# Kernel tuning notes

Measured on AMD Instinct MI355X. Metric: run time of the kernel, lower is better.

Reference implementation:

```python
import jax, jax.numpy as jnp
import numpy as np

N_HEAD = 16


def setup_inputs() -> dict:
    key = jax.random.key(0)
    k1, k2, k3 = jax.random.split(key, 3)
    B, S, D = 4, 2048, 1024
    scale = 1.0 / np.sqrt(D)
    return {
        "inp": jax.random.normal(k1, (B, S, D), dtype=jnp.float32),
        "w_attn": jax.random.normal(k2, (D, 3 * D), dtype=jnp.float32) * scale,
        "b_attn": jnp.zeros((3 * D,), dtype=jnp.float32),
        "w_proj": jax.random.normal(k3, (D, D), dtype=jnp.float32) * scale,
        "b_proj": jnp.zeros((D,), dtype=jnp.float32),
    }


def reference(inp, w_attn, b_attn, w_proj, b_proj):
    B, S, D = inp.shape
    H = N_HEAD
    hd = D // H
    qkv = inp @ w_attn + b_attn                      # [B,S,3D]
    q, k, v = jnp.split(qkv, 3, axis=-1)
    q = q.reshape(B, S, H, hd)
    k = k.reshape(B, S, H, hd)
    v = v.reshape(B, S, H, hd)
    # scores [B,H,S,S], scaled by 1/sqrt(head_dim)
    scores = jnp.einsum("bqhd,bkhd->bhqk", q, k) / jnp.sqrt(jnp.asarray(hd, dtype=inp.dtype))
    # causal mask: position q attends to k <= q
    causal = jnp.tril(jnp.ones((S, S), dtype=bool))
    scores = jnp.where(causal[None, None], scores, jnp.asarray(-jnp.inf, dtype=scores.dtype))
    probs = jax.nn.softmax(scores, axis=-1)          # dropout omitted (eval mode)
    ctx = jnp.einsum("bhqk,bkhd->bqhd", probs, v).reshape(B, S, D)
    return ctx @ w_proj + b_proj
```

## Files before the change

### kernel.cpp

```cpp
#include <hip/hip_runtime.h>


#define DEV __device__ __forceinline__

typedef unsigned short u16;
typedef unsigned u32x4 __attribute__((ext_vector_type(4)));
typedef u16   u16x8 __attribute__((ext_vector_type(8)));
typedef u16   u16x4 __attribute__((ext_vector_type(4)));
typedef float f32x4v __attribute__((ext_vector_type(4)));
typedef __bf16 bf16x8 __attribute__((ext_vector_type(8)));

#define BB 4
#define SS 2048
#define DD 1024
#define HH 16
#define HD 64
#define MM (BB*SS)
#define N3D (3*DD)
#define C8  0.18033688011112042f

DEV u16 f2bf(float f) { return __builtin_bit_cast(u16, (__bf16)f); }
DEV float bf2f(u16 h) { return __builtin_bit_cast(float, (unsigned)h << 16); }

DEV f32x4v mfma16(u16x8 a, u16x8 b, f32x4v c) {
  return __builtin_amdgcn_mfma_f32_16x16x32_bf16(
      __builtin_bit_cast(bf16x8, a), __builtin_bit_cast(bf16x8, b), c, 0, 0, 0);
}

DEV void async16(const void* g, void* l) {
  __builtin_amdgcn_global_load_lds(
      (const __attribute__((address_space(1))) void*)g,
      (__attribute__((address_space(3))) void*)l, 16, 0, 0);
}

__global__ __launch_bounds__(256) void prep_kernel(
    const float* __restrict__ inp, const float* __restrict__ w_attn,
    const float* __restrict__ w_proj, u16* __restrict__ Abf,
    u16* __restrict__ WAt, u16* __restrict__ WPt) {
  const int bid = blockIdx.x;
  const int tid = threadIdx.x;
  if (bid < 4096) {
    __shared__ float t[32][33];
    const float* W; u16* Wt; int N, K, n0, k0;
    if (bid < 3072) { W = w_attn; Wt = WAt; N = N3D; K = DD;
                      n0 = (bid % 96) * 32; k0 = (bid / 96) * 32; }
    else            { W = w_proj; Wt = WPt; N = DD;  K = DD;
                      int tb = bid - 3072; n0 = (tb % 32) * 32; k0 = (tb / 32) * 32; }
    int tx = tid & 31, ty = tid >> 5;
    for (int i = ty; i < 32; i += 8)
      t[i][tx] = W[(long long)(k0 + i) * N + n0 + tx];
    __syncthreads();
    for (int i = ty; i < 32; i += 8)
      Wt[(long long)(n0 + i) * K + k0 + tx] = f2bf(t[tx][i]);
  } else {
    const long long n = (long long)MM * DD;
    long long i = (long long)(bid - 4096) * 256 + tid;
    for (long long j = i * 4; j < n; j += 2048LL * 256 * 4) {
      f32x4v v = *(const f32x4v*)(inp + j);
      u16x4 o;
      o.x = f2bf(v.x); o.y = f2bf(v.y); o.z = f2bf(v.z); o.w = f2bf(v.w);
      *(u16x4*)(Abf + j) = o;
    }
  }
}

__global__ __launch_bounds__(256) void gemm_kernel(
    const u16* __restrict__ A, const u16* __restrict__ Bt,
    const float* __restrict__ bias, void* __restrict__ Cout,
    u16* __restrict__ Vt, int Ndim, int Kdim, int mode) {
  __shared__ __align__(16) char smem[65536];

  const int tid = threadIdx.x;
  const int lane = tid & 63, wid = tid >> 6;
  const int l15 = lane & 15, lg = lane >> 4;

  const int nwg = (int)(gridDim.x * gridDim.y);
  const int orig = (int)(blockIdx.y * gridDim.x + blockIdx.x);
  const int wg = (orig & 7) * (nwg >> 3) + (orig >> 3);
  const int bx = wg % (int)gridDim.x, by = wg / (int)gridDim.x;
  const int rb = by * 128, cb = bx * 128;
  const int wr = (wid >> 1) * 64, wc = (wid & 1) * 64;

  f32x4v acc[4][4] = {};

  const int rlo = tid >> 3;
  const int cbS = (tid & 7) * 16;
  const int swS = cbS ^ ((rlo & 7) << 4);
  const int sd  = rlo * 128 + cbS;

  const int xr  = (l15 & 7) << 4;
  const int vaA = l15 * 128 + ((lg * 16) ^ xr);
  const int gvA0 = wr * 128 + vaA, gvA1 = gvA0 ^ 64;
  const int gvB0 = wc * 128 + vaA, gvB1 = gvB0 ^ 64;

  const char* pa[4];
  const char* pb[4];
#pragma unroll
  for (int i = 0; i < 4; ++i) {
    pa[i] = (const char*)A  + (long long)(rb + i * 32 + rlo) * (Kdim * 2) + swS;
    pb[i] = (const char*)Bt + (long long)(cb + i * 32 + rlo) * (Kdim * 2) + swS;
  }

  auto stage = [&](int dofs, int kb) {
#pragma unroll
    for (int i = 0; i < 4; ++i) {
      async16(pa[i] + kb, smem + dofs + i * 4096 + sd);
      async16(pb[i] + kb, smem + 32768 + dofs + i * 4096 + sd);
    }
  };

  auto compute = [&](int aofs, int bofs) {
    u16x8 a0[4], b0[4], a1[4], b1[4];
#pragma unroll
    for (int mi = 0; mi < 4; ++mi) {
      a0[mi] = *(const u16x8*)(smem + aofs + mi * 2048 + gvA0);
      a1[mi] = *(const u16x8*)(smem + aofs + mi * 2048 + gvA1);
    }
#pragma unroll
    for (int ni = 0; ni < 4; ++ni) {
      b0[ni] = *(const u16x8*)(smem + bofs + ni * 2048 + gvB0);
      b1[ni] = *(const u16x8*)(smem + bofs + ni * 2048 + gvB1);
    }
#pragma unroll
    for (int mi = 0; mi < 4; ++mi)
#pragma unroll
      for (int ni = 0; ni < 4; ++ni) {
        acc[mi][ni] = mfma16(a0[mi], b0[ni], acc[mi][ni]);
        acc[mi][ni] = mfma16(a1[mi], b1[ni], acc[mi][ni]);
      }
  };

  const int nK = Kdim >> 6;
  stage(0, 0);
  __syncthreads();
  for (int kt = 0; kt < nK; kt += 2) {
    stage(16384, 128);
    compute(0, 32768);
    __syncthreads();
    if (kt + 2 < nK) stage(0, 256);
    compute(16384, 49152);
    __syncthreads();
#pragma unroll
    for (int i = 0; i < 4; ++i) { pa[i] += 256; pb[i] += 256; }
  }

#pragma unroll
  for (int mi = 0; mi < 4; ++mi)
#pragma unroll
    for (int ni = 0; ni < 4; ++ni) {
      int col = cb + wc + ni * 16 + l15;
      float bv = bias[col];
      if (mode == 1 && col >= 2 * DD) {
        int h = (col >> 6) & 15, d = col & 63;
#pragma unroll
        for (int r = 0; r < 4; ++r) {
          int row = rb + wr + mi * 16 + lg * 4 + r;
          int b = row >> 11, s = row & 2047;
          Vt[(((long long)(b * HH + h) * HD + d) << 11) + s] = f2bf(acc[mi][ni][r] + bv);
        }
      } else {
#pragma unroll
        for (int r = 0; r < 4; ++r) {
          int row = rb + wr + mi * 16 + lg * 4 + r;
          float v = acc[mi][ni][r] + bv;
          if (mode) ((u16*)Cout)[(long long)row * Ndim + col] = f2bf(v);
          else      ((float*)Cout)[(long long)row * Ndim + col] = v;
        }
      }
    }
}

__global__ __launch_bounds__(512, 4) void attn_kernel(
    const u16* __restrict__ qkv, const u16* __restrict__ Vt,
    u16* __restrict__ ctx) {
  __shared__ __align__(16) char smem[32768];

  const int tid = threadIdx.x, lane = tid & 63, wid = tid >> 6;
  const int l15 = lane & 15, lg = lane >> 4;

  const int orig = (int)blockIdx.x;
  const int wgid = (orig & 7) * 64 + (orig >> 3);
  const int pair = wgid & 7;
  const int bh = wgid >> 3;
  const int b = bh >> 4, h = bh & 15;

  const u16* Qcol = qkv + (long long)b * SS * N3D + h * HD;
  const u16* Kcol = qkv + (long long)b * SS * N3D + DD + h * HD;
  const u16* Vbh  = Vt + (long long)bh * HD * SS;

  const int rowA = 8 * (l15 >> 2) + (l15 & 3);
  const int vk0 = rowA * 128 + ((lg * 16) ^ ((l15 & 3) << 4));
  const int vk1 = vk0 ^ 64;
  const int vk2 = (rowA + 4) * 128 + ((lg * 16) ^ (((l15 & 3) + 4) << 4));
  const int vk3 = vk2 ^ 64;
  const int vv0 = l15 * 128 + ((lg * 16) ^ ((l15 & 7) << 4));
  const int vv1 = vv0 ^ 64;

  const int rlo = tid >> 3;
  const int cbS = (tid & 7) * 16;
  const int swS = cbS ^ ((rlo & 7) << 4);
  const int sd  = rlo * 128 + cbS;
  const long long KSTP = 64LL * N3D * 2;
  const long long VSTP = 64LL * 2;

  auto stage = [&](int dofs, const char* ka, const char* va) {
    async16(ka, smem + dofs + sd);
    async16(va, smem + 16384 + dofs + sd);
  };

#pragma unroll 1
  for (int half = 0; half < 2; ++half) {
    const int qt = half ? pair : 15 - pair;
    const int q0 = qt * 128;
    const int qw = q0 + wid * 16;
    const int nkb = 2 * qt + 2;

    u16x8 qf[2];
#pragma unroll
    for (int kk = 0; kk < 2; ++kk)
      qf[kk] = *(const u16x8*)(Qcol + (long long)(qw + l15) * N3D + kk * 32 + lg * 8);

    f32x4v acc[4] = {};
    float m_s = -1e30f, l_p = 0.f;

    const char* ka = (const char*)Kcol + (long long)rlo * (N3D * 2) + swS;
    const char* va = (const char*)Vbh + (long long)rlo * (SS * 2) + swS;

    auto compute = [&](int kofs, int vofs, int kbase) {
      if (kbase > qw + 15) return;

      f32x4v pf[2][2] = {};
      {
        u16x8 k00 = *(const u16x8*)(smem + kofs + vk0);
        u16x8 k01 = *(const u16x8*)(smem + kofs + vk1);
        u16x8 k10 = *(const u16x8*)(smem + kofs + vk2);
        u16x8 k11 = *(const u16x8*)(smem + kofs + vk3);
        u16x8 k20 = *(const u16x8*)(smem + kofs + 4096 + vk0);
        u16x8 k21 = *(const u16x8*)(smem + kofs + 4096 + vk1);
        u16x8 k30 = *(const u16x8*)(smem + kofs + 4096 + vk2);
        u16x8 k31 = *(const u16x8*)(smem + kofs + 4096 + vk3);
        __builtin_amdgcn_s_setprio(1);
        pf[0][0] = mfma16(k00, qf[0], pf[0][0]);
        pf[0][0] = mfma16(k01, qf[1], pf[0][0]);
        pf[0][1] = mfma16(k10, qf[0], pf[0][1]);
        pf[0][1] = mfma16(k11, qf[1], pf[0][1]);
        pf[1][0] = mfma16(k20, qf[0], pf[1][0]);
        pf[1][0] = mfma16(k21, qf[1], pf[1][0]);
        pf[1][1] = mfma16(k30, qf[0], pf[1][1]);
        pf[1][1] = mfma16(k31, qf[1], pf[1][1]);
        __builtin_amdgcn_s_setprio(0);
      }

      if (kbase + 63 > qw) {
        const int qg = qw + l15;
        const int kl = kbase + lg * 8;
#pragma unroll
        for (int ks = 0; ks < 2; ++ks)
#pragma unroll
          for (int ab = 0; ab < 2; ++ab)
#pragma unroll
            for (int r = 0; r < 4; ++r)
              if (kl + ks * 32 + ab * 4 + r > qg) pf[ks][ab][r] = -1e30f;
      }

      float lmax = pf[0][0][0];
#pragma unroll
      for (int ks = 0; ks < 2; ++ks)
#pragma unroll
        for (int ab = 0; ab < 2; ++ab)
#pragma unroll
          for (int r = 0; r < 4; ++r)
            lmax = fmaxf(lmax, pf[ks][ab][r]);
      if (__any(lmax > m_s + 64.f)) {
        float rm = fmaxf(lmax, __shfl_xor(lmax, 16));
        rm = fmaxf(rm, __shfl_xor(rm, 32));
        float newm = fmaxf(m_s, rm);
        float sc = __builtin_exp2f((m_s - newm) * C8);
        m_s = newm;
        l_p *= sc;
#pragma unroll
        for (int r = 0; r < 4; ++r) {
          float scq = __shfl(sc, (lane & 48) + lg * 4 + r);
#pragma unroll
          for (int di = 0; di < 4; ++di) acc[di][r] *= scq;
        }
      }
      {
        float mC = m_s * C8;
        float rsum = 0.f;
#pragma unroll
        for (int ks = 0; ks < 2; ++ks)
#pragma unroll
          for (int ab = 0; ab < 2; ++ab)
#pragma unroll
            for (int r = 0; r < 4; ++r) {
              float p = __builtin_exp2f(__builtin_fmaf(pf[ks][ab][r], C8, -mC));
              pf[ks][ab][r] = p;
              rsum += p;
            }
        l_p += rsum;
      }

      u32x4 w0, w1;
      w0.x = (unsigned)f2bf(pf[0][0][0]) | ((unsigned)f2bf(pf[0][0][1]) << 16);
      w0.y = (unsigned)f2bf(pf[0][0][2]) | ((unsigned)f2bf(pf[0][0][3]) << 16);
      w0.z = (unsigned)f2bf(pf[0][1][0]) | ((unsigned)f2bf(pf[0][1][1]) << 16);
      w0.w = (unsigned)f2bf(pf[0][1][2]) | ((unsigned)f2bf(pf[0][1][3]) << 16);
      w1.x = (unsigned)f2bf(pf[1][0][0]) | ((unsigned)f2bf(pf[1][0][1]) << 16);
      w1.y = (unsigned)f2bf(pf[1][0][2]) | ((unsigned)f2bf(pf[1][0][3]) << 16);
      w1.z = (unsigned)f2bf(pf[1][1][0]) | ((unsigned)f2bf(pf[1][1][1]) << 16);
      w1.w = (unsigned)f2bf(pf[1][1][2]) | ((unsigned)f2bf(pf[1][1][3]) << 16);
      u16x8 pa0 = __builtin_bit_cast(u16x8, w0);
      u16x8 pa1 = __builtin_bit_cast(u16x8, w1);

      u16x8 v0[4], v1[4];
#pragma unroll
      for (int di = 0; di < 4; ++di) {
        v0[di] = *(const u16x8*)(smem + vofs + di * 2048 + vv0);
        v1[di] = *(const u16x8*)(smem + vofs + di * 2048 + vv1);
      }
      __builtin_amdgcn_s_setprio(1);
#pragma unroll
      for (int di = 0; di < 4; ++di) {
        acc[di] = mfma16(pa0, v0[di], acc[di]);
        acc[di] = mfma16(pa1, v1[di], acc[di]);
      }
      __builtin_amdgcn_s_setprio(0);
    };

    stage(0, ka, va);
    __syncthreads();

    for (int kb = 0; kb < nkb; kb += 2) {
      stage(8192, ka + KSTP, va + VSTP);
      compute(0, 16384, kb * 64);
      __syncthreads();
      if (kb + 2 < nkb) stage(0, ka + 2 * KSTP, va + 2 * VSTP);
      compute(8192, 24576, (kb + 1) * 64);
      __syncthreads();
      ka += 2 * KSTP; va += 2 * VSTP;
    }

    float l_red = l_p + __shfl_xor(l_p, 16);
    l_red += __shfl_xor(l_red, 32);
#pragma unroll
    for (int r = 0; r < 4; ++r) {
      float lq = __shfl(l_red, (lane & 48) + lg * 4 + r);
      float inv = 1.f / lq;
      int qrow = qw + lg * 4 + r;
#pragma unroll
      for (int di = 0; di < 4; ++di) {
        int d = di * 16 + l15;
        ctx[((long long)(b * SS + qrow)) * DD + h * HD + d] = f2bf(acc[di][r] * inv);
      }
    }
  }
}

extern "C" void kernel_launch(void* const* d_in, const int* in_sizes, int n_in,
                              void* d_out, int out_size, void* d_ws, size_t ws_size,
                              hipStream_t stream) {
  const float* inp    = (const float*)d_in[0];
  const float* w_attn = (const float*)d_in[1];
  const float* b_attn = (const float*)d_in[2];
  const float* w_proj = (const float*)d_in[3];
  const float* b_proj = (const float*)d_in[4];
  float* out = (float*)d_out;
  char* ws = (char*)d_ws;

  const long long off_A   = 0;
  const long long off_WAt = 16777216;
  const long long off_WPt = 23068672;
  const long long off_qkv = 25165824;
  const long long off_ctx = 75497472;
  const long long off_Vt  = 92274688;
  const long long need    = 109051904;
  if (ws_size < (size_t)need) return;

  u16* Abf = (u16*)(ws + off_A);
  u16* WAt = (u16*)(ws + off_WAt);
  u16* WPt = (u16*)(ws + off_WPt);
  u16* qkv = (u16*)(ws + off_qkv);
  u16* ctx = (u16*)(ws + off_ctx);
  u16* Vt  = (u16*)(ws + off_Vt);

  prep_kernel<<<6144, 256, 0, stream>>>(inp, w_attn, w_proj, Abf, WAt, WPt);
  gemm_kernel<<<dim3(N3D / 128, MM / 128), 256, 0, stream>>>(
      Abf, WAt, b_attn, qkv, Vt, N3D, DD, 1);
  attn_kernel<<<512, 512, 0, stream>>>(qkv, Vt, ctx);
  gemm_kernel<<<dim3(DD / 128, MM / 128), 256, 0, stream>>>(
      ctx, WPt, b_proj, out, nullptr, DD, DD, 0);
}
```

Measured before the change: 178.1 us.

## Restructure attention to 4-wave blocks with 32 query rows per wave

The attention kernel now runs 256-thread blocks, one per query tile, instead of 512-thread blocks that each looped over two paired tiles. Each wave handles 32 query rows (two 16-row MFMA tiles), so every K and V fragment read from LDS feeds twice as many MFMAs, halving LDS traffic per FLOP. The block-to-work mapping is changed to interleave long and short causal tiles across the grid for load balance, and the LDS swizzle pattern is adjusted. It costs more registers per wave and loses the explicit pairing of long and short tiles inside a block.

```diff
diff --git a/kernel.cpp b/kernel.cpp
--- a/kernel.cpp
+++ b/kernel.cpp
@@ -170,7 +170,7 @@
     }
 }
 
-__global__ __launch_bounds__(512, 4) void attn_kernel(
+__global__ __launch_bounds__(256, 4) void attn_kernel(
     const u16* __restrict__ qkv, const u16* __restrict__ Vt,
     u16* __restrict__ ctx) {
   __shared__ __align__(16) char smem[32768];
@@ -178,10 +178,13 @@
   const int tid = threadIdx.x, lane = tid & 63, wid = tid >> 6;
   const int l15 = lane & 15, lg = lane >> 4;
 
-  const int orig = (int)blockIdx.x;
-  const int wgid = (orig & 7) * 64 + (orig >> 3);
-  const int pair = wgid & 7;
-  const int bh = wgid >> 3;
+  const int d = (int)blockIdx.x;
+  const int rank = d >> 3;
+  const int t = rank >> 3;
+  const int jj = t & 3, q4 = t >> 2;
+  const int qt = (q4 == 0) ? 15 - jj : (q4 == 1) ? 8 + jj
+               : (q4 == 2) ? 7 - jj  : jj;
+  const int bh = (d & 7) * 8 + (rank & 7);
   const int b = bh >> 4, h = bh & 15;
 
   const u16* Qcol = qkv + (long long)b * SS * N3D + h * HD;
@@ -189,169 +192,206 @@
   const u16* Vbh  = Vt + (long long)bh * HD * SS;
 
   const int rowA = 8 * (l15 >> 2) + (l15 & 3);
-  const int vk0 = rowA * 128 + ((lg * 16) ^ ((l15 & 3) << 4));
+  const int kA = (((l15 & 3) | (((l15 >> 2) & 1) << 2))) << 4;
+  const int vk0 = rowA * 128 + ((lg * 16) ^ kA);
   const int vk1 = vk0 ^ 64;
-  const int vk2 = (rowA + 4) * 128 + ((lg * 16) ^ (((l15 & 3) + 4) << 4));
+  const int vk2 = vk0 + 512;
   const int vk3 = vk2 ^ 64;
-  const int vv0 = l15 * 128 + ((lg * 16) ^ ((l15 & 7) << 4));
+  const int kV = (((l15 & 3) | (((l15 >> 3) & 1) << 2))) << 4;
+  const int vv0 = l15 * 128 + ((lg * 16) ^ kV);
   const int vv1 = vv0 ^ 64;
 
   const int rlo = tid >> 3;
   const int cbS = (tid & 7) * 16;
-  const int swS = cbS ^ ((rlo & 7) << 4);
+  const int kw = (((rlo & 3) | (((rlo >> 3) & 1) << 2))) << 4;
+  const int swS = cbS ^ kw;
   const int sd  = rlo * 128 + cbS;
   const long long KSTP = 64LL * N3D * 2;
   const long long VSTP = 64LL * 2;
+  const long long KHLF = 32LL * N3D * 2;
+  const long long VHLF = 32LL * SS * 2;
 
   auto stage = [&](int dofs, const char* ka, const char* va) {
-    async16(ka, smem + dofs + sd);
-    async16(va, smem + 16384 + dofs + sd);
+    async16(ka,        smem + dofs + sd);
+    async16(ka + KHLF, smem + dofs + 4096 + sd);
+    async16(va,        smem + 16384 + dofs + sd);
+    async16(va + VHLF, smem + 16384 + dofs + 4096 + sd);
   };
 
-#pragma unroll 1
-  for (int half = 0; half < 2; ++half) {
-    const int qt = half ? pair : 15 - pair;
-    const int q0 = qt * 128;
-    const int qw = q0 + wid * 16;
-    const int nkb = 2 * qt + 2;
-
-    u16x8 qf[2];
+  const int q0 = qt * 128;
+  const int qw = q0 + wid * 32;
+  const int nkb = 2 * qt + 2;
+
+  u16x8 qf[2][2];
+#pragma unroll
+  for (int mi = 0; mi < 2; ++mi)
 #pragma unroll
     for (int kk = 0; kk < 2; ++kk)
-      qf[kk] = *(const u16x8*)(Qcol + (long long)(qw + l15) * N3D + kk * 32 + lg * 8);
-
-    f32x4v acc[4] = {};
-    float m_s = -1e30f, l_p = 0.f;
-
-    const char* ka = (const char*)Kcol + (long long)rlo * (N3D * 2) + swS;
-    const char* va = (const char*)Vbh + (long long)rlo * (SS * 2) + swS;
-
-    auto compute = [&](int kofs, int vofs, int kbase) {
-      if (kbase > qw + 15) return;
-
-      f32x4v pf[2][2] = {};
-      {
-        u16x8 k00 = *(const u16x8*)(smem + kofs + vk0);
-        u16x8 k01 = *(const u16x8*)(smem + kofs + vk1);
-        u16x8 k10 = *(const u16x8*)(smem + kofs + vk2);
-        u16x8 k11 = *(const u16x8*)(smem + kofs + vk3);
-        u16x8 k20 = *(const u16x8*)(smem + kofs + 4096 + vk0);
-        u16x8 k21 = *(const u16x8*)(smem + kofs + 4096 + vk1);
-        u16x8 k30 = *(const u16x8*)(smem + kofs + 4096 + vk2);
-        u16x8 k31 = *(const u16x8*)(smem + kofs + 4096 + vk3);
-        __builtin_amdgcn_s_setprio(1);
-        pf[0][0] = mfma16(k00, qf[0], pf[0][0]);
-        pf[0][0] = mfma16(k01, qf[1], pf[0][0]);
-        pf[0][1] = mfma16(k10, qf[0], pf[0][1]);
-        pf[0][1] = mfma16(k11, qf[1], pf[0][1]);
-        pf[1][0] = mfma16(k20, qf[0], pf[1][0]);
-        pf[1][0] = mfma16(k21, qf[1], pf[1][0]);
-        pf[1][1] = mfma16(k30, qf[0], pf[1][1]);
-        pf[1][1] = mfma16(k31, qf[1], pf[1][1]);
-        __builtin_amdgcn_s_setprio(0);
-      }
-
-      if (kbase + 63 > qw) {
-        const int qg = qw + l15;
-        const int kl = kbase + lg * 8;
+      qf[mi][kk] = *(const u16x8*)(Qcol + (long long)(qw + mi * 16 + l15) * N3D +
+                                   kk * 32 + lg * 8);
+
+  f32x4v acc[2][4] = {};
+  float m_s[2] = {-1e30f, -1e30f}, l_p[2] = {0.f, 0.f};
+
+  const char* ka = (const char*)Kcol + (long long)rlo * (N3D * 2) + swS;
+  const char* va = (const char*)Vbh + (long long)rlo * (SS * 2) + swS;
+
+  auto compute = [&](int kofs, int vofs, int kbase) {
+    if (kbase > qw + 31) return;
+
+    f32x4v pf[2][2][2] = {};
+    {
+      u16x8 kf0, kf1;
+      kf0 = *(const u16x8*)(smem + kofs + vk0);
+      kf1 = *(const u16x8*)(smem + kofs + vk1);
+      __builtin_amdgcn_s_setprio(1);
+      pf[0][0][0] = mfma16(kf0, qf[0][0], pf[0][0][0]);
+      pf[0][0][0] = mfma16(kf1, qf[0][1], pf[0][0][0]);
+      pf[1][0][0] = mfma16(kf0, qf[1][0], pf[1][0][0]);
+      pf[1][0][0] = mfma16(kf1, qf[1][1], pf[1][0][0]);
+      __builtin_amdgcn_s_setprio(0);
+      kf0 = *(const u16x8*)(smem + kofs + vk2);
+      kf1 = *(const u16x8*)(smem + kofs + vk3);
+      __builtin_amdgcn_s_setprio(1);
+      pf[0][0][1] = mfma16(kf0, qf[0][0], pf[0][0][1]);
+      pf[0][0][1] = mfma16(kf1, qf[0][1], pf[0][0][1]);
+      pf[1][0][1] = mfma16(kf0, qf[1][0], pf[1][0][1]);
+      pf[1][0][1] = mfma16(kf1, qf[1][1], pf[1][0][1]);
+      __builtin_amdgcn_s_setprio(0);
+      kf0 = *(const u16x8*)(smem + kofs + 4096 + vk0);
+      kf1 = *(const u16x8*)(smem + kofs + 4096 + vk1);
+      __builtin_amdgcn_s_setprio(1);
+      pf[0][1][0] = mfma16(kf0, qf[0][0], pf[0][1][0]);
+      pf[0][1][0] = mfma16(kf1, qf[0][1], pf[0][1][0]);
+      pf[1][1][0] = mfma16(kf0, qf[1][0], pf[1][1][0]);
+      pf[1][1][0] = mfma16(kf1, qf[1][1], pf[1][1][0]);
+      __builtin_amdgcn_s_setprio(0);
+      kf0 = *(const u16x8*)(smem + kofs + 4096 + vk2);
+      kf1 = *(const u16x8*)(smem + kofs + 4096 + vk3);
+      __builtin_amdgcn_s_setprio(1);
+      pf[0][1][1] = mfma16(kf0, qf[0][0], pf[0][1][1]);
+      pf[0][1][1] = mfma16(kf1, qf[0][1], pf[0][1][1]);
+      pf[1][1][1] = mfma16(kf0, qf[1][0], pf[1][1][1]);
+      pf[1][1][1] = mfma16(kf1, qf[1][1], pf[1][1][1]);
+      __builtin_amdgcn_s_setprio(0);
+    }
+
+    if (kbase + 63 > qw) {
+      const int kl = kbase + lg * 8;
+#pragma unroll
+      for (int mi = 0; mi < 2; ++mi) {
+        const int qg = qw + mi * 16 + l15;
 #pragma unroll
         for (int ks = 0; ks < 2; ++ks)
 #pragma unroll
           for (int ab = 0; ab < 2; ++ab)
 #pragma unroll
             for (int r = 0; r < 4; ++r)
-              if (kl + ks * 32 + ab * 4 + r > qg) pf[ks][ab][r] = -1e30f;
-      }
-
-      float lmax = pf[0][0][0];
-#pragma unroll
-      for (int ks = 0; ks < 2; ++ks)
-#pragma unroll
-        for (int ab = 0; ab < 2; ++ab)
-#pragma unroll
-          for (int r = 0; r < 4; ++r)
-            lmax = fmaxf(lmax, pf[ks][ab][r]);
-      if (__any(lmax > m_s + 64.f)) {
-        float rm = fmaxf(lmax, __shfl_xor(lmax, 16));
+              if (kl + ks * 32 + ab * 4 + r > qg) pf[mi][ks][ab][r] = -1e30f;
+      }
+    }
+
+    float lmax[2];
+    bool need = false;
+#pragma unroll
+    for (int mi = 0; mi < 2; ++mi) {
+      float v0 = fmaxf(fmaxf(fmaxf(pf[mi][0][0][0], pf[mi][0][0][1]),
+                             pf[mi][0][0][2]), pf[mi][0][0][3]);
+      float v1 = fmaxf(fmaxf(fmaxf(pf[mi][0][1][0], pf[mi][0][1][1]),
+                             pf[mi][0][1][2]), pf[mi][0][1][3]);
+      float v2 = fmaxf(fmaxf(fmaxf(pf[mi][1][0][0], pf[mi][1][0][1]),
+                             pf[mi][1][0][2]), pf[mi][1][0][3]);
+      float v3 = fmaxf(fmaxf(fmaxf(pf[mi][1][1][0], pf[mi][1][1][1]),
+                             pf[mi][1][1][2]), pf[mi][1][1][3]);
+      lmax[mi] = fmaxf(fmaxf(v0, v1), fmaxf(v2, v3));
+      need = need || (lmax[mi] > m_s[mi] + 64.f);
+    }
+    if (__any(need)) {
+#pragma unroll
+      for (int mi = 0; mi < 2; ++mi) {
+        float rm = fmaxf(lmax[mi], __shfl_xor(lmax[mi], 16));
         rm = fmaxf(rm, __shfl_xor(rm, 32));
-        float newm = fmaxf(m_s, rm);
-        float sc = __builtin_exp2f((m_s - newm) * C8);
-        m_s = newm;
-        l_p *= sc;
+        float newm = fmaxf(m_s[mi], rm);
+        float sc = __builtin_exp2f((m_s[mi] - newm) * C8);
+        m_s[mi] = newm;
+        l_p[mi] *= sc;
 #pragma unroll
         for (int r = 0; r < 4; ++r) {
           float scq = __shfl(sc, (lane & 48) + lg * 4 + r);
 #pragma unroll
-          for (int di = 0; di < 4; ++di) acc[di][r] *= scq;
+          for (int di = 0; di < 4; ++di) acc[mi][di][r] *= scq;
         }
       }
-      {
-        float mC = m_s * C8;
-        float rsum = 0.f;
-#pragma unroll
-        for (int ks = 0; ks < 2; ++ks)
-#pragma unroll
-          for (int ab = 0; ab < 2; ++ab)
-#pragma unroll
-            for (int r = 0; r < 4; ++r) {
-              float p = __builtin_exp2f(__builtin_fmaf(pf[ks][ab][r], C8, -mC));
-              pf[ks][ab][r] = p;
-              rsum += p;
-            }
-        l_p += rsum;
-      }
-
-      u32x4 w0, w1;
-      w0.x = (unsigned)f2bf(pf[0][0][0]) | ((unsigned)f2bf(pf[0][0][1]) << 16);
-      w0.y = (unsigned)f2bf(pf[0][0][2]) | ((unsigned)f2bf(pf[0][0][3]) << 16);
-      w0.z = (unsigned)f2bf(pf[0][1][0]) | ((unsigned)f2bf(pf[0][1][1]) << 16);
-      w0.w = (unsigned)f2bf(pf[0][1][2]) | ((unsigned)f2bf(pf[0][1][3]) << 16);
-      w1.x = (unsigned)f2bf(pf[1][0][0]) | ((unsigned)f2bf(pf[1][0][1]) << 16);
-      w1.y = (unsigned)f2bf(pf[1][0][2]) | ((unsigned)f2bf(pf[1][0][3]) << 16);
-      w1.z = (unsigned)f2bf(pf[1][1][0]) | ((unsigned)f2bf(pf[1][1][1]) << 16);
-      w1.w = (unsigned)f2bf(pf[1][1][2]) | ((unsigned)f2bf(pf[1][1][3]) << 16);
-      u16x8 pa0 = __builtin_bit_cast(u16x8, w0);
-      u16x8 pa1 = __builtin_bit_cast(u16x8, w1);
-
-      u16x8 v0[4], v1[4];
-#pragma unroll
-      for (int di = 0; di < 4; ++di) {
-        v0[di] = *(const u16x8*)(smem + vofs + di * 2048 + vv0);
-        v1[di] = *(const u16x8*)(smem + vofs + di * 2048 + vv1);
-      }
+    }
+#pragma unroll
+    for (int mi = 0; mi < 2; ++mi) {
+      float mC = m_s[mi] * C8;
+      float rsum = 0.f;
+#pragma unroll
+      for (int ks = 0; ks < 2; ++ks)
+#pragma unroll
+        for (int ab = 0; ab < 2; ++ab)
+#pragma unroll
+          for (int r = 0; r < 4; ++r) {
+            float p = __builtin_exp2f(__builtin_fmaf(pf[mi][ks][ab][r], C8, -mC));
+            pf[mi][ks][ab][r] = p;
+            rsum += p;
+          }
+      l_p[mi] += rsum;
+    }
+
+    u16x8 pa[2][2];
+#pragma unroll
+    for (int mi = 0; mi < 2; ++mi)
+#pragma unroll
+      for (int ks = 0; ks < 2; ++ks) {
+        u32x4 w;
+        w.x = (unsigned)f2bf(pf[mi][ks][0][0]) | ((unsigned)f2bf(pf[mi][ks][0][1]) << 16);
+        w.y = (unsigned)f2bf(pf[mi][ks][0][2]) | ((unsigned)f2bf(pf[mi][ks][0][3]) << 16);
+        w.z = (unsigned)f2bf(pf[mi][ks][1][0]) | ((unsigned)f2bf(pf[mi][ks][1][1]) << 16);
+        w.w = (unsigned)f2bf(pf[mi][ks][1][2]) | ((unsigned)f2bf(pf[mi][ks][1][3]) << 16);
+        pa[mi][ks] = __builtin_bit_cast(u16x8, w);
+      }
+
+#pragma unroll
+    for (int di = 0; di < 4; ++di) {
+      u16x8 v0 = *(const u16x8*)(smem + vofs + di * 2048 + vv0);
+      u16x8 v1 = *(const u16x8*)(smem + vofs + di * 2048 + vv1);
       __builtin_amdgcn_s_setprio(1);
-#pragma unroll
-      for (int di = 0; di < 4; ++di) {
-        acc[di] = mfma16(pa0, v0[di], acc[di]);
-        acc[di] = mfma16(pa1, v1[di], acc[di]);
-      }
+      acc[0][di] = mfma16(pa[0][0], v0, acc[0][di]);
+      acc[0][di] = mfma16(pa[0][1], v1, acc[0][di]);
+      acc[1][di] = mfma16(pa[1][0], v0, acc[1][di]);
+      acc[1][di] = mfma16(pa[1][1], v1, acc[1][di]);
       __builtin_amdgcn_s_setprio(0);
-    };
-
-    stage(0, ka, va);
+    }
+  };
+
+  stage(0, ka, va);
+  __syncthreads();
+
+  for (int kb = 0; kb < nkb; kb += 2) {
+    stage(8192, ka + KSTP, va + VSTP);
+    compute(0, 16384, kb * 64);
     __syncthreads();
-
-    for (int kb = 0; kb < nkb; kb += 2) {
-      stage(8192, ka + KSTP, va + VSTP);
-      compute(0, 16384, kb * 64);
-      __syncthreads();
-      if (kb + 2 < nkb) stage(0, ka + 2 * KSTP, va + 2 * VSTP);
-      compute(8192, 24576, (kb + 1) * 64);
-      __syncthreads();
-      ka += 2 * KSTP; va += 2 * VSTP;
-    }
-
-    float l_red = l_p + __shfl_xor(l_p, 16);
+    if (kb + 2 < nkb) stage(0, ka + 2 * KSTP, va + 2 * VSTP);
+    compute(8192, 24576, (kb + 1) * 64);
+    __syncthreads();
+    ka += 2 * KSTP; va += 2 * VSTP;
+  }
+
+#pragma unroll
+  for (int mi = 0; mi < 2; ++mi) {
+    float l_red = l_p[mi] + __shfl_xor(l_p[mi], 16);
     l_red += __shfl_xor(l_red, 32);
 #pragma unroll
     for (int r = 0; r < 4; ++r) {
       float lq = __shfl(l_red, (lane & 48) + lg * 4 + r);
       float inv = 1.f / lq;
-      int qrow = qw + lg * 4 + r;
+      int qrow = qw + mi * 16 + lg * 4 + r;
 #pragma unroll
       for (int di = 0; di < 4; ++di) {
-        int d = di * 16 + l15;
-        ctx[((long long)(b * SS + qrow)) * DD + h * HD + d] = f2bf(acc[di][r] * inv);
+        int dd = di * 16 + l15;
+        ctx[((long long)(b * SS + qrow)) * DD + h * HD + dd] = f2bf(acc[mi][di][r] * inv);
       }
     }
   }
@@ -387,7 +427,7 @@
   prep_kernel<<<6144, 256, 0, stream>>>(inp, w_attn, w_proj, Abf, WAt, WPt);
   gemm_kernel<<<dim3(N3D / 128, MM / 128), 256, 0, stream>>>(
       Abf, WAt, b_attn, qkv, Vt, N3D, DD, 1);
-  attn_kernel<<<512, 512, 0, stream>>>(qkv, Vt, ctx);
+  attn_kernel<<<1024, 256, 0, stream>>>(qkv, Vt, ctx);
   gemm_kernel<<<dim3(DD / 128, MM / 128), 256, 0, stream>>>(
       ctx, WPt, b_proj, out, nullptr, DD, DD, 0);
 }
```

Result: no change. 175.5 us (-1.5%).
